# Optimization experiments

Hardware: AMD Instinct MI355X
Metric: run time of the kernel (lower is better)

Reference implementation:

```python
import jax, jax.numpy as jnp
import numpy as np

P = 8  # patch size
EPS = 1e-6

def ln2d(x, w, b):
    # LayerNorm over channel dim (dim=1), biased variance
    m = x.mean(1, keepdims=True)
    v = jnp.var(x, axis=1, keepdims=True)
    return (x - m) / jnp.sqrt(v + EPS) * w + b

def conv1x1(x, w, b=None):
    y = jnp.einsum('bchw,oc->bohw', x, w)
    if b is not None:
        y = y + b[None, :, None, None]
    return y

def dwconv3(x, w):
    # depthwise 3x3, padding=1; w: (C,1,3,3)
    return jax.lax.conv_general_dilated(
        x, w, window_strides=(1, 1), padding='SAME',
        feature_group_count=x.shape[1],
        dimension_numbers=('NCHW', 'OIHW', 'NCHW'))

def to_patches(x):
    B, C, H, W = x.shape
    x = x.reshape(B, C, H // P, P, W // P, P)
    return x.transpose(0, 1, 2, 4, 3, 5)  # b c h w p1 p2

def from_patches(x):
    B, C, h, w, p1, p2 = x.shape
    return x.transpose(0, 1, 2, 4, 3, 5).reshape(B, C, h * p1, w * p2)

def setup_inputs() -> dict:
    key = jax.random.key(0)
    ks = jax.random.split(key, 20)
    dim = 128
    dw = dim * 2          # 256
    ffn = dim * 2         # 256
    B, H, W = 2, 256, 256
    s = lambda k, shape, scale=0.05: jax.random.normal(k, shape, jnp.float32) * scale
    return {
        'x': jax.random.normal(ks[0], (B, dim, H, W), jnp.float32),
        'norm1_w': jnp.ones((1, dim, 1, 1), jnp.float32),
        'norm1_b': jnp.zeros((1, dim, 1, 1), jnp.float32),
        'w_h1': s(ks[1], (dw * 3, dim)),
        'w_dw1': s(ks[2], (dw * 3, 1, 3, 3)),
        'norm2_w': jnp.ones((1, dw, 1, 1), jnp.float32),
        'norm2_b': jnp.zeros((1, dw, 1, 1), jnp.float32),
        'w_p1': s(ks[3], (dim, dw)),
        'norm3_w': jnp.ones((1, dim, 1, 1), jnp.float32),
        'norm3_b': jnp.zeros((1, dim, 1, 1), jnp.float32),
        'w_h2': s(ks[4], (ffn, dim)),
        'b_h2': s(ks[5], (ffn,)),
        'w_dw2': s(ks[6], (ffn, 1, 3, 3)),
        'w_p2': s(ks[7], (dim, ffn // 2)),
        'scale1': s(ks[8], (1, dim, 1, 1), 0.01),
        'scale2': s(ks[9], (1, dim, 1, 1), 0.01),
    }

def reference(x, norm1_w, norm1_b, w_h1, w_dw1, norm2_w, norm2_b, w_p1,
              norm3_w, norm3_b, w_h2, b_h2, w_dw2, w_p2, scale1, scale2):
    identity = x
    h = ln2d(x, norm1_w, norm1_b)
    hidden = conv1x1(h, w_h1)
    qkv = dwconv3(hidden, w_dw1)
    q, k, v = jnp.split(qkv, 3, axis=1)
    # patch-wise FFT attention
    q_fft = jnp.fft.rfft2(to_patches(q).astype(jnp.float32), axes=(-2, -1))
    k_fft = jnp.fft.rfft2(to_patches(k).astype(jnp.float32), axes=(-2, -1))
    attn = jnp.fft.irfft2(q_fft * k_fft, s=(P, P), axes=(-2, -1))
    attn = from_patches(attn)
    attn = ln2d(attn, norm2_w, norm2_b)
    out = conv1x1(v * attn, w_p1)
    x = identity + out * scale1
    # FFN branch
    identity = x
    h = ln2d(x, norm3_w, norm3_b)
    h = conv1x1(h, w_h2, b_h2)
    h = dwconv3(h, w_dw2)
    h1, h2 = jnp.split(h, 2, axis=1)
    h = conv1x1(h1 * h2, w_p2)
    return identity + h * scale2
```

## Files before the change

kernel.cpp:

```cpp
#include <hip/hip_runtime.h>

typedef unsigned short u16;
typedef unsigned int u32;
typedef __attribute__((ext_vector_type(8))) short bf16x8;
typedef __attribute__((ext_vector_type(4))) float f32x4;

#define HW 65536

__device__ __forceinline__ float bf2f(u32 v) { return __uint_as_float(v << 16); }
__device__ __forceinline__ u16 f2bf(float f) {
  u32 u = __float_as_uint(f);
  u += 0x7fffu + ((u >> 16) & 1u);
  return (u16)(u >> 16);
}

__device__ __forceinline__ float dot2bf(u32 a, u32 b, float d) {
  asm("v_dot2_f32_bf16 %0, %1, %2, %0" : "+v"(d) : "v"(a), "v"(b));
  return d;
}

__device__ __forceinline__ void unpack8(uint4 u, float r[8]) {
  r[0] = bf2f(u.x & 0xffffu); r[1] = bf2f(u.x >> 16);
  r[2] = bf2f(u.y & 0xffffu); r[3] = bf2f(u.y >> 16);
  r[4] = bf2f(u.z & 0xffffu); r[5] = bf2f(u.z >> 16);
  r[6] = bf2f(u.w & 0xffffu); r[7] = bf2f(u.w >> 16);
}

__global__ __launch_bounds__(256)
void wprep_k(const float* __restrict__ wh1, const float* __restrict__ wp1,
             const float* __restrict__ wh2, u16* __restrict__ S)
{
  int i = blockIdx.x * 256 + threadIdx.x;
  if (i < 98304) {
    int j = i & 7, row = (i >> 3) & 127, kc = (i >> 10) & 15, mt = i >> 14;
    S[i] = f2bf(wh1[(mt * 128 + row) * 128 + kc * 8 + j]);
  } else if (i < 131072) {
    int k = i - 98304;
    int j = k & 7, row = (k >> 3) & 127, chl = (k >> 10) & 3, c0c = k >> 12;
    S[i] = f2bf(wp1[row * 256 + c0c * 32 + chl * 8 + j]);
  } else if (i < 163840) {
    int k = i - 131072;
    int j = k & 7, row = (k >> 3) & 127, kc = (k >> 10) & 15, mt = k >> 14;
    S[i] = f2bf(wh2[(mt * 128 + row) * 128 + kc * 8 + j]);
  }
}

__global__ __launch_bounds__(256, 2)
void ln1_k(const float* __restrict__ x, const float* __restrict__ gw,
           const float* __restrict__ gb, u16* __restrict__ y)
{
  __shared__ float xt[128][128];
  __shared__ float stm[128], str[128];
  int n0g = blockIdx.x << 7;
  int b = n0g >> 16;
  int p0 = n0g & (HW - 1);
  const float* xb = x + (size_t)b * 128 * HW + p0;
  u16* yb = y + (size_t)b * 128 * HW + p0;
  int t = threadIdx.x;
#pragma unroll
  for (int it = 0; it < 16; ++it) {
    int idx = t + it * 256;
    int ch = idx >> 5;
    int p4 = (idx & 31) << 2;
    *(float4*)&xt[ch][p4] = *(const float4*)(xb + (size_t)ch * HW + p4);
  }
  __syncthreads();
  if (t < 128) {
    float s = 0.f, q = 0.f;
    for (int c = 0; c < 128; ++c) {
      float a = xt[c][t];
      s += a; q += a * a;
    }
    const float inv = 1.0f / 128.0f;
    float m = s * inv;
    stm[t] = m;
    str[t] = rsqrtf(fmaxf(q * inv - m * m, 0.f) + 1e-6f);
  }
  __syncthreads();
  int p2 = (t & 63) << 1;
  int c0 = t >> 6;
  float m0 = stm[p2], r0 = str[p2], m1 = stm[p2 + 1], r1 = str[p2 + 1];
#pragma unroll
  for (int k = 0; k < 32; ++k) {
    int c = c0 + k * 4;
    float w = gw[c], bb = gb[c];
    float a = (xt[c][p2] - m0) * r0 * w + bb;
    float d = (xt[c][p2 + 1] - m1) * r1 * w + bb;
    *(u32*)(yb + (size_t)c * HW + p2) = (u32)f2bf(a) | ((u32)f2bf(d) << 16);
  }
}

__device__ __forceinline__ void gatherB(const u16* __restrict__ src,
                                        uint4& e, uint4& o)
{
  u32 w0 = *(const u32*)(src);
  u32 w1 = *(const u32*)(src + HW);
  u32 w2 = *(const u32*)(src + 2 * HW);
  u32 w3 = *(const u32*)(src + 3 * HW);
  u32 w4 = *(const u32*)(src + 4 * HW);
  u32 w5 = *(const u32*)(src + 5 * HW);
  u32 w6 = *(const u32*)(src + 6 * HW);
  u32 w7 = *(const u32*)(src + 7 * HW);
  e.x = (w0 & 0xffffu) | (w1 << 16);
  e.y = (w2 & 0xffffu) | (w3 << 16);
  e.z = (w4 & 0xffffu) | (w5 << 16);
  e.w = (w6 & 0xffffu) | (w7 << 16);
  o.x = (w0 >> 16) | (w1 & 0xffff0000u);
  o.y = (w2 >> 16) | (w3 & 0xffff0000u);
  o.z = (w4 >> 16) | (w5 & 0xffff0000u);
  o.w = (w6 >> 16) | (w7 & 0xffff0000u);
}

template <int AUXF32, int OUTF32>
__global__ __launch_bounds__(256, 2)
void gemm_k(const float* __restrict__ Wt, const u16* __restrict__ X,
            void* __restrict__ Yv, const void* __restrict__ aux,
            const float* __restrict__ scale, int M, int K, int xbatch)
{
  __shared__ __align__(16) u16 As[4][128][8];
  __shared__ __align__(16) u16 Bs[4][128][8];
  int mtiles = M >> 7;
  int mt = blockIdx.x % mtiles;
  int ntile = blockIdx.x / mtiles;
  int n0g = ntile << 7;
  int b = n0g >> 16;
  int p0 = n0g & (HW - 1);
  int o0 = mt << 7;
  const u16* Xb = X + (size_t)b * xbatch * HW;
  int t = threadIdx.x;
  int lane = t & 63, wv = t >> 6;
  int rb = (wv & 1) << 6, cb = (wv >> 1) << 6;
  int qd = lane >> 4, ln = lane & 15;
  f32x4 acc[4][4] = {};
  for (int c0 = 0; c0 < K; c0 += 32) {
#pragma unroll
    for (int it = 0; it < 2; ++it) {
      int tt = t + it * 256;
      int row = tt >> 2, ch = tt & 3;
      const float* wsrc = Wt + (size_t)(o0 + row) * K + c0 + ch * 8;
      uint4 pk;
      pk.x = (u32)f2bf(wsrc[0]) | ((u32)f2bf(wsrc[1]) << 16);
      pk.y = (u32)f2bf(wsrc[2]) | ((u32)f2bf(wsrc[3]) << 16);
      pk.z = (u32)f2bf(wsrc[4]) | ((u32)f2bf(wsrc[5]) << 16);
      pk.w = (u32)f2bf(wsrc[6]) | ((u32)f2bf(wsrc[7]) << 16);
      *(uint4*)&As[ch][row][0] = pk;
    }
    {
      int pp = (t & 63) << 1;
      int kc = t >> 6;
      const u16* src = Xb + (size_t)(c0 + kc * 8) * HW + p0 + pp;
      uint4 e, o;
      gatherB(src, e, o);
      *(uint4*)&Bs[kc][pp][0] = e;
      *(uint4*)&Bs[kc][pp + 1][0] = o;
    }
    __syncthreads();
    bf16x8 af[4], bfv[4];
#pragma unroll
    for (int i = 0; i < 4; ++i) {
      af[i] = *(const bf16x8*)&As[qd][rb + i * 16 + ln][0];
      bfv[i] = *(const bf16x8*)&Bs[qd][cb + i * 16 + ln][0];
    }
#pragma unroll
    for (int i = 0; i < 4; ++i)
#pragma unroll
      for (int j = 0; j < 4; ++j)
        acc[i][j] = __builtin_amdgcn_mfma_f32_16x16x32_bf16(af[i], bfv[j],
                                                            acc[i][j], 0, 0, 0);
    __syncthreads();
  }
  size_t ybase = (size_t)b * M * HW;
#pragma unroll
  for (int i = 0; i < 4; ++i) {
    int obase = o0 + rb + i * 16 + qd * 4;
#pragma unroll
    for (int j = 0; j < 4; ++j) {
      int p = p0 + cb + j * 16 + ln;
#pragma unroll
      for (int rr = 0; rr < 4; ++rr) {
        int o = obase + rr;
        size_t idx = ybase + (size_t)o * HW + p;
        float v = acc[i][j][rr];
        float r = AUXF32 ? ((const float*)aux)[idx]
                         : bf2f((u32)((const u16*)aux)[idx]);
        v = r + v * scale[o];
        if (OUTF32) ((float*)Yv)[idx] = v;
        else        ((u16*)Yv)[idx] = f2bf(v);
      }
    }
  }
}

__global__ __launch_bounds__(256, 2)
void lngemm_k(const u16* __restrict__ Wbf, const u16* __restrict__ X,
              u16* __restrict__ Y, const float* __restrict__ aux,
              const float* __restrict__ scale, const float* __restrict__ gw,
              const float* __restrict__ gb)
{
  __shared__ __align__(16) u16 At[32][128][8];
  __shared__ __align__(16) u16 As[4][128][8];
  __shared__ float stm[128], str[128];
  int n0g = blockIdx.x << 7;
  int b = n0g >> 16;
  int p0 = n0g & (HW - 1);
  const u16* Xb = X + (size_t)b * 768 * HW;
  int t = threadIdx.x;
  int lane = t & 63, wv = t >> 6;
  int rb = (wv & 1) << 6, cb = (wv >> 1) << 6;
  int qd = lane >> 4, ln = lane & 15;
#pragma unroll
  for (int it = 0; it < 8; ++it) {
    int kc = (t >> 6) + it * 4;
    int pp = (t & 63) << 1;
    const u16* src = Xb + (size_t)(kc * 8) * HW + p0 + pp;
    uint4 e, o;
    gatherB(src, e, o);
    *(uint4*)&At[kc][pp][0] = e;
    *(uint4*)&At[kc][pp + 1][0] = o;
  }
  __syncthreads();
  if (t < 128) {
    float s0 = 0.f, q0 = 0.f;
    for (int cg = 0; cg < 128; ++cg) {
      u32 u = *(const u32*)&At[cg >> 2][t][(cg & 3) << 1];
      float a = bf2f(u & 0xffffu);
      s0 += a; q0 += a * a;
      float d = bf2f(u >> 16);
      s0 += d; q0 += d * d;
    }
    const float inv = 1.0f / 256.0f;
    float m0 = s0 * inv;
    stm[t] = m0;
    str[t] = rsqrtf(fmaxf(q0 * inv - m0 * m0, 0.f) + 1e-6f);
  }
  __syncthreads();
  f32x4 acc[4][4] = {};
  for (int c0 = 0; c0 < 256; c0 += 32) {
    {
      const uint4* wsrc = (const uint4*)(Wbf + (size_t)(c0 >> 5) * 4096);
      ((uint4*)As)[t] = wsrc[t];
      ((uint4*)As)[t + 256] = wsrc[t + 256];
    }
    {
      int kcg = (c0 >> 3) + (t >> 6);
      int pp = (t & 63) << 1;
      const u16* vsrc = Xb + (size_t)(512 + kcg * 8) * HW + p0 + pp;
      uint4 ve, vo;
      gatherB(vsrc, ve, vo);
      float w8[8], b8[8];
#pragma unroll
      for (int j = 0; j < 8; ++j) {
        w8[j] = gw[kcg * 8 + j];
        b8[j] = gb[kcg * 8 + j];
      }
      float m0 = stm[pp], r0 = str[pp];
      float m1 = stm[pp + 1], r1 = str[pp + 1];
      uint4 e = *(const uint4*)&At[kcg][pp][0];
      uint4 o = *(const uint4*)&At[kcg][pp + 1][0];
      const u32* ew = (const u32*)&e;
      const u32* ow = (const u32*)&o;
      const u32* vew = (const u32*)&ve;
      const u32* vow = (const u32*)&vo;
      u32 re[4], ro[4];
#pragma unroll
      for (int j = 0; j < 4; ++j) {
        float a0 = ((bf2f(ew[j] & 0xffffu) - m0) * r0 * w8[2 * j] + b8[2 * j]) *
                   bf2f(vew[j] & 0xffffu);
        float a1 = ((bf2f(ew[j] >> 16) - m0) * r0 * w8[2 * j + 1] + b8[2 * j + 1]) *
                   bf2f(vew[j] >> 16);
        re[j] = (u32)f2bf(a0) | ((u32)f2bf(a1) << 16);
        float d0 = ((bf2f(ow[j] & 0xffffu) - m1) * r1 * w8[2 * j] + b8[2 * j]) *
                   bf2f(vow[j] & 0xffffu);
        float d1 = ((bf2f(ow[j] >> 16) - m1) * r1 * w8[2 * j + 1] + b8[2 * j + 1]) *
                   bf2f(vow[j] >> 16);
        ro[j] = (u32)f2bf(d0) | ((u32)f2bf(d1) << 16);
      }
      *(uint4*)&At[kcg][pp][0] = *(const uint4*)re;
      *(uint4*)&At[kcg][pp + 1][0] = *(const uint4*)ro;
    }
    __syncthreads();
    bf16x8 af[4], bfv[4];
    int kb = c0 >> 3;
#pragma unroll
    for (int i = 0; i < 4; ++i) {
      af[i] = *(const bf16x8*)&As[qd][rb + i * 16 + ln][0];
      bfv[i] = *(const bf16x8*)&At[kb + qd][cb + i * 16 + ln][0];
    }
#pragma unroll
    for (int i = 0; i < 4; ++i)
#pragma unroll
      for (int j = 0; j < 4; ++j)
        acc[i][j] = __builtin_amdgcn_mfma_f32_16x16x32_bf16(af[i], bfv[j],
                                                            acc[i][j], 0, 0, 0);
    __syncthreads();
  }
  size_t ybase = (size_t)b * 128 * HW;
#pragma unroll
  for (int i = 0; i < 4; ++i) {
    int obase = rb + i * 16 + qd * 4;
#pragma unroll
    for (int j = 0; j < 4; ++j) {
      int p = p0 + cb + j * 16 + ln;
#pragma unroll
      for (int rr = 0; rr < 4; ++rr) {
        int o = obase + rr;
        size_t idx = ybase + (size_t)o * HW + p;
        float v = acc[i][j][rr];
        float r = aux[idx];
        Y[idx] = f2bf(r + v * scale[o]);
      }
    }
  }
}

template <int EPI>
__global__ __launch_bounds__(256, 2)
void gemmf_k(const u16* __restrict__ Wbf, const u16* __restrict__ X,
             u16* __restrict__ Y, const float* __restrict__ bias,
             int MT, int xbatch)
{
  __shared__ __align__(16) u16 Bs[16][128][8];
  __shared__ __align__(16) u16 As[16][128][8];
  int n0g = blockIdx.x << 7;
  int b = n0g >> 16;
  int p0 = n0g & (HW - 1);
  const u16* Xb = X + (size_t)b * xbatch * HW;
  int t = threadIdx.x;
  int lane = t & 63, wv = t >> 6;
  int rb = (wv & 1) << 6, cb = (wv >> 1) << 6;
  int qd = lane >> 4, ln = lane & 15;
#pragma unroll
  for (int it = 0; it < 4; ++it) {
    int tt = t + it * 256;
    int pp = (tt & 63) << 1;
    int kc = tt >> 6;
    const u16* src = Xb + (size_t)(kc * 8) * HW + p0 + pp;
    uint4 e, o;
    gatherB(src, e, o);
    *(uint4*)&Bs[kc][pp][0] = e;
    *(uint4*)&Bs[kc][pp + 1][0] = o;
  }
  int M = MT << 7;
  size_t ybase = (size_t)b * M * HW;
  for (int mt = 0; mt < MT; ++mt) {
    __syncthreads();
    {
      const uint4* wsrc = (const uint4*)(Wbf + (size_t)mt * 16384);
#pragma unroll
      for (int it = 0; it < 8; ++it)
        ((uint4*)As)[t + it * 256] = wsrc[t + it * 256];
    }
    __syncthreads();
    f32x4 acc[4][4] = {};
#pragma unroll
    for (int s = 0; s < 4; ++s) {
      bf16x8 af[4], bfv[4];
#pragma unroll
      for (int i = 0; i < 4; ++i) {
        af[i] = *(const bf16x8*)&As[s * 4 + qd][rb + i * 16 + ln][0];
        bfv[i] = *(const bf16x8*)&Bs[s * 4 + qd][cb + i * 16 + ln][0];
      }
#pragma unroll
      for (int i = 0; i < 4; ++i)
#pragma unroll
        for (int j = 0; j < 4; ++j)
          acc[i][j] = __builtin_amdgcn_mfma_f32_16x16x32_bf16(af[i], bfv[j],
                                                              acc[i][j], 0, 0, 0);
    }
    int o0 = mt << 7;
#pragma unroll
    for (int i = 0; i < 4; ++i) {
      int obase = o0 + rb + i * 16 + qd * 4;
#pragma unroll
      for (int j = 0; j < 4; ++j) {
        int p = p0 + cb + j * 16 + ln;
#pragma unroll
        for (int rr = 0; rr < 4; ++rr) {
          int o = obase + rr;
          float v = acc[i][j][rr];
          if (EPI == 1) v += bias[o];
          Y[ybase + (size_t)o * HW + p] = f2bf(v);
        }
      }
    }
  }
}

__global__ __launch_bounds__(256, 2)
void lngemmf_k(const u16* __restrict__ Wbf, const u16* __restrict__ X,
               u16* __restrict__ Y, const float* __restrict__ bias,
               const float* __restrict__ gw, const float* __restrict__ gb,
               int MT, int xbatch)
{
  __shared__ __align__(16) u16 Bs[16][128][8];
  __shared__ __align__(16) u16 As[16][128][8];
  __shared__ float stm[128], str[128];
  int n0g = blockIdx.x << 7;
  int b = n0g >> 16;
  int p0 = n0g & (HW - 1);
  const u16* Xb = X + (size_t)b * xbatch * HW;
  int t = threadIdx.x;
  int lane = t & 63, wv = t >> 6;
  int rb = (wv & 1) << 6, cb = (wv >> 1) << 6;
  int qd = lane >> 4, ln = lane & 15;
#pragma unroll
  for (int it = 0; it < 4; ++it) {
    int tt = t + it * 256;
    int pp = (tt & 63) << 1;
    int kc = tt >> 6;
    const u16* src = Xb + (size_t)(kc * 8) * HW + p0 + pp;
    uint4 e, o;
    gatherB(src, e, o);
    *(uint4*)&Bs[kc][pp][0] = e;
    *(uint4*)&Bs[kc][pp + 1][0] = o;
  }
  __syncthreads();
  if (t < 128) {
    float s = 0.f, q = 0.f;
    for (int kc = 0; kc < 16; ++kc) {
      float r8[8];
      unpack8(*(const uint4*)&Bs[kc][t][0], r8);
#pragma unroll
      for (int j = 0; j < 8; ++j) {
        float a = r8[j];
        s += a; q += a * a;
      }
    }
    const float inv = 1.0f / 128.0f;
    float m = s * inv;
    stm[t] = m;
    str[t] = rsqrtf(fmaxf(q * inv - m * m, 0.f) + 1e-6f);
  }
  __syncthreads();
  {
    int pp = (t & 63) << 1;
    float m0 = stm[pp], r0 = str[pp];
    float m1 = stm[pp + 1], r1 = str[pp + 1];
#pragma unroll
    for (int mth = 0; mth < 4; ++mth) {
      int kc = (t >> 6) + mth * 4;
      float w8[8], b8[8];
#pragma unroll
      for (int j = 0; j < 8; ++j) {
        w8[j] = gw[kc * 8 + j];
        b8[j] = gb[kc * 8 + j];
      }
      float e8[8], o8[8];
      unpack8(*(const uint4*)&Bs[kc][pp][0], e8);
      unpack8(*(const uint4*)&Bs[kc][pp + 1][0], o8);
      uint4 pe, po;
      u32* pew = (u32*)&pe;
      u32* pow = (u32*)&po;
#pragma unroll
      for (int j = 0; j < 4; ++j) {
        float a0 = (e8[2 * j] - m0) * r0 * w8[2 * j] + b8[2 * j];
        float a1 = (e8[2 * j + 1] - m0) * r0 * w8[2 * j + 1] + b8[2 * j + 1];
        pew[j] = (u32)f2bf(a0) | ((u32)f2bf(a1) << 16);
        float d0 = (o8[2 * j] - m1) * r1 * w8[2 * j] + b8[2 * j];
        float d1 = (o8[2 * j + 1] - m1) * r1 * w8[2 * j + 1] + b8[2 * j + 1];
        pow[j] = (u32)f2bf(d0) | ((u32)f2bf(d1) << 16);
      }
      *(uint4*)&Bs[kc][pp][0] = pe;
      *(uint4*)&Bs[kc][pp + 1][0] = po;
    }
  }
  int M = MT << 7;
  size_t ybase = (size_t)b * M * HW;
  for (int mt = 0; mt < MT; ++mt) {
    __syncthreads();
    {
      const uint4* wsrc = (const uint4*)(Wbf + (size_t)mt * 16384);
#pragma unroll
      for (int it = 0; it < 8; ++it)
        ((uint4*)As)[t + it * 256] = wsrc[t + it * 256];
    }
    __syncthreads();
    f32x4 acc[4][4] = {};
#pragma unroll
    for (int s = 0; s < 4; ++s) {
      bf16x8 af[4], bfv[4];
#pragma unroll
      for (int i = 0; i < 4; ++i) {
        af[i] = *(const bf16x8*)&As[s * 4 + qd][rb + i * 16 + ln][0];
        bfv[i] = *(const bf16x8*)&Bs[s * 4 + qd][cb + i * 16 + ln][0];
      }
#pragma unroll
      for (int i = 0; i < 4; ++i)
#pragma unroll
        for (int j = 0; j < 4; ++j)
          acc[i][j] = __builtin_amdgcn_mfma_f32_16x16x32_bf16(af[i], bfv[j],
                                                              acc[i][j], 0, 0, 0);
    }
    int o0 = mt << 7;
#pragma unroll
    for (int i = 0; i < 4; ++i) {
      int obase = o0 + rb + i * 16 + qd * 4;
#pragma unroll
      for (int j = 0; j < 4; ++j) {
        int p = p0 + cb + j * 16 + ln;
#pragma unroll
        for (int rr = 0; rr < 4; ++rr) {
          int o = obase + rr;
          Y[ybase + (size_t)o * HW + p] = f2bf(acc[i][j][rr] + bias[o]);
        }
      }
    }
  }
}

__device__ __forceinline__ void ldsrow(const u16* __restrict__ img, int h,
                                       int w0, float* r) {
  if ((unsigned)h > 255u) {
#pragma unroll
    for (int i = 0; i < 10; ++i) r[i] = 0.f;
    return;
  }
  const u16* rp = img + (h << 8) + w0;
  float c[8];
  unpack8(*(const uint4*)rp, c);
#pragma unroll
  for (int i = 0; i < 8; ++i) r[i + 1] = c[i];
  r[0] = (w0 > 0) ? bf2f((u32)rp[-1]) : 0.f;
  r[9] = (w0 < 248) ? bf2f((u32)rp[8]) : 0.f;
}

__global__ __launch_bounds__(1024)
void dwip_k(u16* __restrict__ buf, const float* __restrict__ wt, int C)
{
  __shared__ __align__(16) u16 img[65536];
  int bc = blockIdx.x;
  int c = bc % C;
  size_t base = (size_t)bc << 16;
  int t = threadIdx.x;
  uint4* simg = (uint4*)img;
  const uint4* gsrc = (const uint4*)(buf + base);
#pragma unroll
  for (int it = 0; it < 8; ++it)
    simg[it * 1024 + t] = gsrc[it * 1024 + t];
  float wg[9];
#pragma unroll
  for (int i = 0; i < 9; ++i) wg[i] = wt[c * 9 + i];
  __syncthreads();
  uint4* gdst = (uint4*)(buf + base);
  int col = t & 31;
  int w0 = col << 3;
  int h0 = (t >> 5) << 3;
  float r0[10], r1[10], r2[10];
  ldsrow(img, h0 - 1, w0, r0);
  ldsrow(img, h0,     w0, r1);
#pragma unroll
  for (int k = 0; k < 8; ++k) {
    int h = h0 + k;
    ldsrow(img, h + 1, w0, r2);
    float o[8];
#pragma unroll
    for (int j = 0; j < 8; ++j) {
      float s = 0.f;
#pragma unroll
      for (int dx = 0; dx < 3; ++dx)
        s += r0[j + dx] * wg[dx] + r1[j + dx] * wg[3 + dx] +
             r2[j + dx] * wg[6 + dx];
      o[j] = s;
    }
    uint4 pk;
    pk.x = (u32)f2bf(o[0]) | ((u32)f2bf(o[1]) << 16);
    pk.y = (u32)f2bf(o[2]) | ((u32)f2bf(o[3]) << 16);
    pk.z = (u32)f2bf(o[4]) | ((u32)f2bf(o[5]) << 16);
    pk.w = (u32)f2bf(o[6]) | ((u32)f2bf(o[7]) << 16);
    gdst[(h << 5) + col] = pk;
#pragma unroll
    for (int i = 0; i < 10; ++i) { r0[i] = r1[i]; r1[i] = r2[i]; }
  }
}

__device__ __forceinline__ void ldsrow2(const u16* __restrict__ img, int lr,
                                        int w0, float* r) {
  const u16* rp = img + (lr << 8) + w0;
  float c[8];
  unpack8(*(const uint4*)rp, c);
#pragma unroll
  for (int i = 0; i < 8; ++i) r[i + 1] = c[i];
  r[0] = (w0 > 0) ? bf2f((u32)rp[-1]) : 0.f;
  r[9] = (w0 < 248) ? bf2f((u32)rp[8]) : 0.f;
}

__global__ __launch_bounds__(1024)
void dwfuse_k(const u16* __restrict__ h4, const float* __restrict__ wt,
              u16* __restrict__ pr)
{
  __shared__ __align__(16) u16 img[33280];
  int bx = blockIdx.x;
  int b = bx >> 8;
  int c = (bx >> 1) & 127;
  int half = bx & 1;
  int h0 = half << 7;
  int t = threadIdx.x;
  float o1[32];
  size_t obase = ((size_t)((b << 7) + c) << 16);
  int col = t & 31;
  int w0 = col << 3;
  int l0 = (t >> 5) << 2;
#pragma unroll
  for (int pass = 0; pass < 2; ++pass) {
    int ch = c + pass * 128;
    size_t gbase = (size_t)((b << 8) + ch) << 16;
    __syncthreads();
    for (int idx = t; idx < 4160; idx += 1024) {
      int lr = idx >> 5, cl = idx & 31;
      int gh = h0 - 1 + lr;
      uint4 v = {0, 0, 0, 0};
      if ((unsigned)gh < 256u)
        v = *(const uint4*)(h4 + gbase + ((size_t)gh << 8) + cl * 8);
      *(uint4*)&img[(lr << 8) + cl * 8] = v;
    }
    float wg[9];
#pragma unroll
    for (int i = 0; i < 9; ++i) wg[i] = wt[ch * 9 + i];
    __syncthreads();
    float r0[10], r1[10], r2[10];
    ldsrow2(img, l0,     w0, r0);
    ldsrow2(img, l0 + 1, w0, r1);
#pragma unroll
    for (int k = 0; k < 4; ++k) {
      int lrr = l0 + k;
      ldsrow2(img, lrr + 2, w0, r2);
      float o[8];
#pragma unroll
      for (int j = 0; j < 8; ++j) {
        float s = 0.f;
#pragma unroll
        for (int dx = 0; dx < 3; ++dx)
          s += r0[j + dx] * wg[dx] + r1[j + dx] * wg[3 + dx] +
               r2[j + dx] * wg[6 + dx];
        o[j] = s;
      }
      if (pass == 0) {
#pragma unroll
        for (int j = 0; j < 8; ++j) o1[k * 8 + j] = o[j];
      } else {
        uint4 pk;
        pk.x = (u32)f2bf(o1[k*8+0] * o[0]) | ((u32)f2bf(o1[k*8+1] * o[1]) << 16);
        pk.y = (u32)f2bf(o1[k*8+2] * o[2]) | ((u32)f2bf(o1[k*8+3] * o[3]) << 16);
        pk.z = (u32)f2bf(o1[k*8+4] * o[4]) | ((u32)f2bf(o1[k*8+5] * o[5]) << 16);
        pk.w = (u32)f2bf(o1[k*8+6] * o[6]) | ((u32)f2bf(o1[k*8+7] * o[7]) << 16);
        *(uint4*)(pr + obase + ((size_t)(h0 + lrr) << 8) + w0) = pk;
      }
#pragma unroll
      for (int i = 0; i < 10; ++i) { r0[i] = r1[i]; r1[i] = r2[i]; }
    }
  }
}

__global__ __launch_bounds__(256)
void attn_k(u16* __restrict__ qkv)
{
  int wv = threadIdx.x >> 6, lane = threadIdx.x & 63;
  int task = blockIdx.x * 4 + wv;
  int b = task >> 12;
  int c = (task >> 4) & 255;
  int strip = task & 15;
  int pr = lane >> 5, pw = lane & 31;
  int row = (strip << 4) + (pr << 3);
  size_t qbase = ((size_t)(b * 768 + c) << 16) + ((size_t)row << 8) + pw * 8;
  size_t kbase = qbase + ((size_t)256 << 16);
  u32 qp[8][4];
  u32 ku[8][4];
#pragma unroll
  for (int i = 0; i < 8; ++i) {
    uint4 qv = *(const uint4*)(qkv + qbase + (i << 8));
    uint4 kv = *(const uint4*)(qkv + kbase + (i << 8));
    qp[i][0] = qv.x; qp[i][1] = qv.y; qp[i][2] = qv.z; qp[i][3] = qv.w;
    ku[i][0] = kv.x; ku[i][1] = kv.y; ku[i][2] = kv.z; ku[i][3] = kv.w;
  }
  u32 pk[8][8];
#pragma unroll
  for (int r = 0; r < 8; ++r)
#pragma unroll
    for (int n = 0; n < 8; ++n) {
      if (n & 1) {
        u32 x = ku[r][n >> 1];
        pk[r][n] = (x >> 16) | (x << 16);
      } else {
        pk[r][n] = (ku[r][n >> 1] & 0xffffu) |
                   (ku[r][((n + 7) & 7) >> 1] & 0xffff0000u);
      }
    }
#pragma unroll
  for (int m = 0; m < 8; ++m) {
    float a[8] = {};
#pragma unroll
    for (int i = 0; i < 8; ++i) {
      const int r = (m - i) & 7;
#pragma unroll
      for (int t = 0; t < 4; ++t) {
        const u32 q = qp[i][t];
#pragma unroll
        for (int n = 0; n < 8; ++n)
          a[n] = dot2bf(q, pk[r][(n - 2 * t) & 7], a[n]);
      }
    }
    uint4 pko;
    pko.x = (u32)f2bf(a[0]) | ((u32)f2bf(a[1]) << 16);
    pko.y = (u32)f2bf(a[2]) | ((u32)f2bf(a[3]) << 16);
    pko.z = (u32)f2bf(a[4]) | ((u32)f2bf(a[5]) << 16);
    pko.w = (u32)f2bf(a[6]) | ((u32)f2bf(a[7]) << 16);
    *(uint4*)(qkv + qbase + (m << 8)) = pko;
  }
}

extern "C" void kernel_launch(void* const* d_in, const int* in_sizes, int n_in,
                              void* d_out, int out_size, void* d_ws, size_t ws_size,
                              hipStream_t stream)
{
  (void)in_sizes; (void)n_in; (void)out_size; (void)ws_size;
  const float* x    = (const float*)d_in[0];
  const float* n1w  = (const float*)d_in[1];
  const float* n1b  = (const float*)d_in[2];
  const float* wh1  = (const float*)d_in[3];
  const float* wdw1 = (const float*)d_in[4];
  const float* n2w  = (const float*)d_in[5];
  const float* n2b  = (const float*)d_in[6];
  const float* wp1  = (const float*)d_in[7];
  const float* n3w  = (const float*)d_in[8];
  const float* n3b  = (const float*)d_in[9];
  const float* wh2  = (const float*)d_in[10];
  const float* bh2  = (const float*)d_in[11];
  const float* wdw2 = (const float*)d_in[12];
  const float* wp2  = (const float*)d_in[13];
  const float* sc1  = (const float*)d_in[14];
  const float* sc2  = (const float*)d_in[15];
  float* out = (float*)d_out;
  u16* ws = (u16*)d_ws;

  u16* A = ws;
  u16* B = ws + 100663296;
  u16* h4 = A + 16777216;
  u16* pr = A;
  u16* S = (u16*)d_out;

  wprep_k<<<640, 256, 0, stream>>>(wh1, wp1, wh2, S);
  ln1_k<<<1024, 256, 0, stream>>>(x, n1w, n1b, B);
  gemmf_k<0><<<1024, 256, 0, stream>>>(S, B, A, nullptr, 6, 128);
  dwip_k<<<1536, 1024, 0, stream>>>(A, wdw1, 768);
  attn_k<<<2048, 256, 0, stream>>>(A);
  lngemm_k<<<1024, 256, 0, stream>>>(S + 98304, A, B, x, sc1, n2w, n2b);
  lngemmf_k<<<1024, 256, 0, stream>>>(S + 131072, B, h4, bh2, n3w, n3b, 2, 128);
  dwfuse_k<<<512, 1024, 0, stream>>>(h4, wdw2, pr);
  gemm_k<0,1><<<1024, 256, 0, stream>>>(wp2, pr, out, B, sc2, 128, 128, 128);
}
```

Baseline: 454.2 us.

## Halve dwconv LDS footprint and pre-convert final GEMM weights to bf16

```diff
diff --git a/kernel.cpp b/kernel.cpp
--- a/kernel.cpp
+++ b/kernel.cpp
@@ -43,6 +43,14 @@
     int j = k & 7, row = (k >> 3) & 127, kc = (k >> 10) & 15, mt = k >> 14;
     S[i] = f2bf(wh2[(mt * 128 + row) * 128 + kc * 8 + j]);
   }
+}
+
+__global__ __launch_bounds__(256)
+void wprep2_k(const float* __restrict__ wp2, u16* __restrict__ S3)
+{
+  int i = blockIdx.x * 256 + threadIdx.x;
+  int j = i & 7, row = (i >> 3) & 127, chl = (i >> 10) & 3, c0c = i >> 12;
+  S3[i] = f2bf(wp2[row * 128 + c0c * 32 + chl * 8 + j]);
 }
 
 __global__ __launch_bounds__(256, 2)
@@ -111,39 +119,27 @@
   o.w = (w6 >> 16) | (w7 & 0xffff0000u);
 }
 
-template <int AUXF32, int OUTF32>
 __global__ __launch_bounds__(256, 2)
-void gemm_k(const float* __restrict__ Wt, const u16* __restrict__ X,
-            void* __restrict__ Yv, const void* __restrict__ aux,
-            const float* __restrict__ scale, int M, int K, int xbatch)
+void gemmw_k(const u16* __restrict__ Wbf, const u16* __restrict__ X,
+             float* __restrict__ Y, const u16* __restrict__ aux,
+             const float* __restrict__ scale)
 {
   __shared__ __align__(16) u16 As[4][128][8];
   __shared__ __align__(16) u16 Bs[4][128][8];
-  int mtiles = M >> 7;
-  int mt = blockIdx.x % mtiles;
-  int ntile = blockIdx.x / mtiles;
-  int n0g = ntile << 7;
+  int n0g = blockIdx.x << 7;
   int b = n0g >> 16;
   int p0 = n0g & (HW - 1);
-  int o0 = mt << 7;
-  const u16* Xb = X + (size_t)b * xbatch * HW;
+  const u16* Xb = X + (size_t)b * 128 * HW;
   int t = threadIdx.x;
   int lane = t & 63, wv = t >> 6;
   int rb = (wv & 1) << 6, cb = (wv >> 1) << 6;
   int qd = lane >> 4, ln = lane & 15;
   f32x4 acc[4][4] = {};
-  for (int c0 = 0; c0 < K; c0 += 32) {
-#pragma unroll
-    for (int it = 0; it < 2; ++it) {
-      int tt = t + it * 256;
-      int row = tt >> 2, ch = tt & 3;
-      const float* wsrc = Wt + (size_t)(o0 + row) * K + c0 + ch * 8;
-      uint4 pk;
-      pk.x = (u32)f2bf(wsrc[0]) | ((u32)f2bf(wsrc[1]) << 16);
-      pk.y = (u32)f2bf(wsrc[2]) | ((u32)f2bf(wsrc[3]) << 16);
-      pk.z = (u32)f2bf(wsrc[4]) | ((u32)f2bf(wsrc[5]) << 16);
-      pk.w = (u32)f2bf(wsrc[6]) | ((u32)f2bf(wsrc[7]) << 16);
-      *(uint4*)&As[ch][row][0] = pk;
+  for (int c0 = 0; c0 < 128; c0 += 32) {
+    {
+      const uint4* wsrc = (const uint4*)(Wbf + (size_t)(c0 >> 5) * 4096);
+      ((uint4*)As)[t] = wsrc[t];
+      ((uint4*)As)[t + 256] = wsrc[t + 256];
     }
     {
       int pp = (t & 63) << 1;
@@ -169,10 +165,10 @@
                                                             acc[i][j], 0, 0, 0);
     __syncthreads();
   }
-  size_t ybase = (size_t)b * M * HW;
+  size_t ybase = (size_t)b * 128 * HW;
 #pragma unroll
   for (int i = 0; i < 4; ++i) {
-    int obase = o0 + rb + i * 16 + qd * 4;
+    int obase = rb + i * 16 + qd * 4;
 #pragma unroll
     for (int j = 0; j < 4; ++j) {
       int p = p0 + cb + j * 16 + ln;
@@ -180,12 +176,8 @@
       for (int rr = 0; rr < 4; ++rr) {
         int o = obase + rr;
         size_t idx = ybase + (size_t)o * HW + p;
-        float v = acc[i][j][rr];
-        float r = AUXF32 ? ((const float*)aux)[idx]
-                         : bf2f((u32)((const u16*)aux)[idx]);
-        v = r + v * scale[o];
-        if (OUTF32) ((float*)Yv)[idx] = v;
-        else        ((u16*)Yv)[idx] = f2bf(v);
+        float r = bf2f((u32)aux[idx]);
+        Y[idx] = r + acc[i][j][rr] * scale[o];
       }
     }
   }
@@ -508,14 +500,14 @@
   }
 }
 
-__device__ __forceinline__ void ldsrow(const u16* __restrict__ img, int h,
-                                       int w0, float* r) {
-  if ((unsigned)h > 255u) {
+__device__ __forceinline__ void ldsrowS(const u16* __restrict__ img, int slot,
+                                        int w0, float* r) {
+  if (slot < 0) {
 #pragma unroll
     for (int i = 0; i < 10; ++i) r[i] = 0.f;
     return;
   }
-  const u16* rp = img + (h << 8) + w0;
+  const u16* rp = img + (slot << 8) + w0;
   float c[8];
   unpack8(*(const uint4*)rp, c);
 #pragma unroll
@@ -524,52 +516,97 @@
   r[9] = (w0 < 248) ? bf2f((u32)rp[8]) : 0.f;
 }
 
+__device__ __forceinline__ int smap(int g) {
+  return (g == 127) ? 127 : (g == 128) ? 128 : g - 129;
+}
+
 __global__ __launch_bounds__(1024)
 void dwip_k(u16* __restrict__ buf, const float* __restrict__ wt, int C)
 {
-  __shared__ __align__(16) u16 img[65536];
+  __shared__ __align__(16) uint4 sl[4128];
+  const u16* L = (const u16*)sl;
   int bc = blockIdx.x;
   int c = bc % C;
-  size_t base = (size_t)bc << 16;
   int t = threadIdx.x;
-  uint4* simg = (uint4*)img;
-  const uint4* gsrc = (const uint4*)(buf + base);
-#pragma unroll
-  for (int it = 0; it < 8; ++it)
-    simg[it * 1024 + t] = gsrc[it * 1024 + t];
   float wg[9];
 #pragma unroll
   for (int i = 0; i < 9; ++i) wg[i] = wt[c * 9 + i];
-  __syncthreads();
-  uint4* gdst = (uint4*)(buf + base);
+  uint4* Gch = (uint4*)(buf + ((size_t)bc << 16));
+  for (int idx = t; idx < 4128; idx += 1024)
+    sl[idx] = Gch[idx];
+  __syncthreads();
+  uint4 st[4];
+#pragma unroll
+  for (int r = 0; r < 4; ++r) {
+    int idx = t + r * 1024;
+    if (idx < 4064) st[r] = Gch[4128 + idx];
+  }
   int col = t & 31;
   int w0 = col << 3;
-  int h0 = (t >> 5) << 3;
-  float r0[10], r1[10], r2[10];
-  ldsrow(img, h0 - 1, w0, r0);
-  ldsrow(img, h0,     w0, r1);
-#pragma unroll
-  for (int k = 0; k < 8; ++k) {
-    int h = h0 + k;
-    ldsrow(img, h + 1, w0, r2);
-    float o[8];
-#pragma unroll
-    for (int j = 0; j < 8; ++j) {
-      float s = 0.f;
-#pragma unroll
-      for (int dx = 0; dx < 3; ++dx)
-        s += r0[j + dx] * wg[dx] + r1[j + dx] * wg[3 + dx] +
-             r2[j + dx] * wg[6 + dx];
-      o[j] = s;
-    }
-    uint4 pk;
-    pk.x = (u32)f2bf(o[0]) | ((u32)f2bf(o[1]) << 16);
-    pk.y = (u32)f2bf(o[2]) | ((u32)f2bf(o[3]) << 16);
-    pk.z = (u32)f2bf(o[4]) | ((u32)f2bf(o[5]) << 16);
-    pk.w = (u32)f2bf(o[6]) | ((u32)f2bf(o[7]) << 16);
-    gdst[(h << 5) + col] = pk;
-#pragma unroll
-    for (int i = 0; i < 10; ++i) { r0[i] = r1[i]; r1[i] = r2[i]; }
+  int h0 = (t >> 5) << 2;
+  {
+    float r0[10], r1[10], r2[10];
+    ldsrowS(L, h0 - 1, w0, r0);
+    ldsrowS(L, h0, w0, r1);
+#pragma unroll
+    for (int k = 0; k < 4; ++k) {
+      int h = h0 + k;
+      ldsrowS(L, h + 1, w0, r2);
+      float o[8];
+#pragma unroll
+      for (int j = 0; j < 8; ++j) {
+        float s = 0.f;
+#pragma unroll
+        for (int dx = 0; dx < 3; ++dx)
+          s += r0[j + dx] * wg[dx] + r1[j + dx] * wg[3 + dx] +
+               r2[j + dx] * wg[6 + dx];
+        o[j] = s;
+      }
+      uint4 pk;
+      pk.x = (u32)f2bf(o[0]) | ((u32)f2bf(o[1]) << 16);
+      pk.y = (u32)f2bf(o[2]) | ((u32)f2bf(o[3]) << 16);
+      pk.z = (u32)f2bf(o[4]) | ((u32)f2bf(o[5]) << 16);
+      pk.w = (u32)f2bf(o[6]) | ((u32)f2bf(o[7]) << 16);
+      Gch[(h << 5) + col] = pk;
+#pragma unroll
+      for (int i = 0; i < 10; ++i) { r0[i] = r1[i]; r1[i] = r2[i]; }
+    }
+  }
+  __syncthreads();
+#pragma unroll
+  for (int r = 0; r < 4; ++r) {
+    int idx = t + r * 1024;
+    if (idx < 4064) sl[idx] = st[r];
+  }
+  __syncthreads();
+  {
+    int R0 = 128 + h0;
+    float r0[10], r1[10], r2[10];
+    ldsrowS(L, smap(R0 - 1), w0, r0);
+    ldsrowS(L, smap(R0), w0, r1);
+#pragma unroll
+    for (int k = 0; k < 4; ++k) {
+      int R = R0 + k;
+      ldsrowS(L, (R == 255) ? -1 : smap(R + 1), w0, r2);
+      float o[8];
+#pragma unroll
+      for (int j = 0; j < 8; ++j) {
+        float s = 0.f;
+#pragma unroll
+        for (int dx = 0; dx < 3; ++dx)
+          s += r0[j + dx] * wg[dx] + r1[j + dx] * wg[3 + dx] +
+               r2[j + dx] * wg[6 + dx];
+        o[j] = s;
+      }
+      uint4 pk;
+      pk.x = (u32)f2bf(o[0]) | ((u32)f2bf(o[1]) << 16);
+      pk.y = (u32)f2bf(o[2]) | ((u32)f2bf(o[3]) << 16);
+      pk.z = (u32)f2bf(o[4]) | ((u32)f2bf(o[5]) << 16);
+      pk.w = (u32)f2bf(o[6]) | ((u32)f2bf(o[7]) << 16);
+      Gch[(R << 5) + col] = pk;
+#pragma unroll
+      for (int i = 0; i < 10; ++i) { r0[i] = r1[i]; r1[i] = r2[i]; }
+    }
   }
 }
 
@@ -737,6 +774,7 @@
   u16* h4 = A + 16777216;
   u16* pr = A;
   u16* S = (u16*)d_out;
+  u16* S3 = A + 16777216;
 
   wprep_k<<<640, 256, 0, stream>>>(wh1, wp1, wh2, S);
   ln1_k<<<1024, 256, 0, stream>>>(x, n1w, n1b, B);
@@ -746,5 +784,6 @@
   lngemm_k<<<1024, 256, 0, stream>>>(S + 98304, A, B, x, sc1, n2w, n2b);
   lngemmf_k<<<1024, 256, 0, stream>>>(S + 131072, B, h4, bh2, n3w, n3b, 2, 128);
   dwfuse_k<<<512, 1024, 0, stream>>>(h4, wdw2, pr);
-  gemm_k<0,1><<<1024, 256, 0, stream>>>(wp2, pr, out, B, sc2, 128, 128, 128);
-}
+  wprep2_k<<<64, 256, 0, stream>>>(wp2, S3);
+  gemmw_k<<<1024, 256, 0, stream>>>(S3, pr, out, B, sc2);
+}
```

After: 498.8 us. 9.8% more time.

## Fuse q/k depthwise conv with patch FFT-attention in one kernel

Applied to the files above, without the earlier changes.

```diff
diff --git a/kernel.cpp b/kernel.cpp
--- a/kernel.cpp
+++ b/kernel.cpp
@@ -43,6 +43,18 @@
     int j = k & 7, row = (k >> 3) & 127, kc = (k >> 10) & 15, mt = k >> 14;
     S[i] = f2bf(wh2[(mt * 128 + row) * 128 + kc * 8 + j]);
   }
+}
+
+__global__ __launch_bounds__(256)
+void qhalo_k(const u16* __restrict__ A, u16* __restrict__ Hq)
+{
+  int i = blockIdx.x * 256 + threadIdx.x;
+  int ch = i >> 6;
+  int off = i & 63;
+  int b = ch >> 8, cq = ch & 255;
+  const uint4* src = (const uint4*)(A + ((size_t)(b * 768 + cq) << 16) +
+                                    (127 << 8));
+  ((uint4*)Hq)[i] = src[off];
 }
 
 __global__ __launch_bounds__(256, 2)
@@ -508,6 +520,17 @@
   }
 }
 
+__device__ __forceinline__ void ldsrow2(const u16* __restrict__ img, int lr,
+                                        int w0, float* r) {
+  const u16* rp = img + (lr << 8) + w0;
+  float c[8];
+  unpack8(*(const uint4*)rp, c);
+#pragma unroll
+  for (int i = 0; i < 8; ++i) r[i + 1] = c[i];
+  r[0] = (w0 > 0) ? bf2f((u32)rp[-1]) : 0.f;
+  r[9] = (w0 < 248) ? bf2f((u32)rp[8]) : 0.f;
+}
+
 __device__ __forceinline__ void ldsrow(const u16* __restrict__ img, int h,
                                        int w0, float* r) {
   if ((unsigned)h > 255u) {
@@ -525,12 +548,13 @@
 }
 
 __global__ __launch_bounds__(1024)
-void dwip_k(u16* __restrict__ buf, const float* __restrict__ wt, int C)
+void dwipv_k(u16* __restrict__ buf, const float* __restrict__ wt)
 {
   __shared__ __align__(16) u16 img[65536];
-  int bc = blockIdx.x;
-  int c = bc % C;
-  size_t base = (size_t)bc << 16;
+  int bx = blockIdx.x;
+  int b = bx >> 8;
+  int c = 512 + (bx & 255);
+  size_t base = (size_t)(b * 768 + c) << 16;
   int t = threadIdx.x;
   uint4* simg = (uint4*)img;
   const uint4* gsrc = (const uint4*)(buf + base);
@@ -573,15 +597,143 @@
   }
 }
 
-__device__ __forceinline__ void ldsrow2(const u16* __restrict__ img, int lr,
-                                        int w0, float* r) {
-  const u16* rp = img + (lr << 8) + w0;
-  float c[8];
-  unpack8(*(const uint4*)rp, c);
-#pragma unroll
-  for (int i = 0; i < 8; ++i) r[i + 1] = c[i];
-  r[0] = (w0 > 0) ? bf2f((u32)rp[-1]) : 0.f;
-  r[9] = (w0 < 248) ? bf2f((u32)rp[8]) : 0.f;
+__global__ __launch_bounds__(1024)
+void qkattn_k(u16* __restrict__ A, const float* __restrict__ wt,
+              const u16* __restrict__ Hq)
+{
+  __shared__ __align__(16) u16 qin[33280];
+  __shared__ __align__(16) u16 kin[33280];
+  int bx = blockIdx.x;
+  int b = bx >> 9;
+  int c = (bx >> 1) & 255;
+  int half = bx & 1;
+  int h0 = half << 7;
+  int t = threadIdx.x;
+  u16* Gq = A + ((size_t)(b * 768 + c) << 16);
+  const u16* Gk = A + ((size_t)(b * 768 + 256 + c) << 16);
+  const u16* Hc = Hq + ((size_t)(b * 256 + c) << 9);
+  for (int idx = t; idx < 4160; idx += 1024) {
+    int lr = idx >> 5, cl = idx & 31;
+    int gh = h0 - 1 + lr;
+    uint4 qv = {0, 0, 0, 0}, kv = {0, 0, 0, 0};
+    if ((unsigned)gh < 256u) {
+      bool other = (half == 0) ? (gh == 128) : (gh == 127);
+      if (other) qv = *(const uint4*)(Hc + ((gh - 127) << 8) + cl * 8);
+      else       qv = *(const uint4*)(Gq + ((size_t)gh << 8) + cl * 8);
+      kv = *(const uint4*)(Gk + ((size_t)gh << 8) + cl * 8);
+    }
+    *(uint4*)&qin[(lr << 8) + cl * 8] = qv;
+    *(uint4*)&kin[(lr << 8) + cl * 8] = kv;
+  }
+  float wq[9], wk[9];
+#pragma unroll
+  for (int i = 0; i < 9; ++i) {
+    wq[i] = wt[c * 9 + i];
+    wk[i] = wt[(256 + c) * 9 + i];
+  }
+  __syncthreads();
+  int col = t & 31, w0 = col << 3, l0 = (t >> 5) << 2;
+  uint4 qres[4], kres[4];
+  {
+    float r0[10], r1[10], r2[10];
+    ldsrow2(qin, l0,     w0, r0);
+    ldsrow2(qin, l0 + 1, w0, r1);
+#pragma unroll
+    for (int kk = 0; kk < 4; ++kk) {
+      ldsrow2(qin, l0 + 2 + kk, w0, r2);
+      float o[8];
+#pragma unroll
+      for (int j = 0; j < 8; ++j) {
+        float s = 0.f;
+#pragma unroll
+        for (int dx = 0; dx < 3; ++dx)
+          s += r0[j + dx] * wq[dx] + r1[j + dx] * wq[3 + dx] +
+               r2[j + dx] * wq[6 + dx];
+        o[j] = s;
+      }
+      qres[kk].x = (u32)f2bf(o[0]) | ((u32)f2bf(o[1]) << 16);
+      qres[kk].y = (u32)f2bf(o[2]) | ((u32)f2bf(o[3]) << 16);
+      qres[kk].z = (u32)f2bf(o[4]) | ((u32)f2bf(o[5]) << 16);
+      qres[kk].w = (u32)f2bf(o[6]) | ((u32)f2bf(o[7]) << 16);
+#pragma unroll
+      for (int i = 0; i < 10; ++i) { r0[i] = r1[i]; r1[i] = r2[i]; }
+    }
+  }
+  {
+    float r0[10], r1[10], r2[10];
+    ldsrow2(kin, l0,     w0, r0);
+    ldsrow2(kin, l0 + 1, w0, r1);
+#pragma unroll
+    for (int kk = 0; kk < 4; ++kk) {
+      ldsrow2(kin, l0 + 2 + kk, w0, r2);
+      float o[8];
+#pragma unroll
+      for (int j = 0; j < 8; ++j) {
+        float s = 0.f;
+#pragma unroll
+        for (int dx = 0; dx < 3; ++dx)
+          s += r0[j + dx] * wk[dx] + r1[j + dx] * wk[3 + dx] +
+               r2[j + dx] * wk[6 + dx];
+        o[j] = s;
+      }
+      kres[kk].x = (u32)f2bf(o[0]) | ((u32)f2bf(o[1]) << 16);
+      kres[kk].y = (u32)f2bf(o[2]) | ((u32)f2bf(o[3]) << 16);
+      kres[kk].z = (u32)f2bf(o[4]) | ((u32)f2bf(o[5]) << 16);
+      kres[kk].w = (u32)f2bf(o[6]) | ((u32)f2bf(o[7]) << 16);
+#pragma unroll
+      for (int i = 0; i < 10; ++i) { r0[i] = r1[i]; r1[i] = r2[i]; }
+    }
+  }
+  __syncthreads();
+  uint4* qc = (uint4*)qin;
+  uint4* kc = (uint4*)kin;
+#pragma unroll
+  for (int kk = 0; kk < 4; ++kk) {
+    qc[((l0 + kk) << 5) + col] = qres[kk];
+    kc[((l0 + kk) << 5) + col] = kres[kk];
+  }
+  __syncthreads();
+  int patch = t >> 1, mh = t & 1;
+  int pr = patch >> 5, pc = patch & 31;
+  u32 qp[8][4];
+  u32 pk[8][8];
+#pragma unroll
+  for (int i = 0; i < 8; ++i) {
+    uint4 qv = qc[((pr * 8 + i) << 5) + pc];
+    qp[i][0] = qv.x; qp[i][1] = qv.y; qp[i][2] = qv.z; qp[i][3] = qv.w;
+    uint4 kv = kc[((pr * 8 + i) << 5) + pc];
+    u32 k0 = kv.x, k1 = kv.y, k2 = kv.z, k3 = kv.w;
+    pk[i][0] = (k0 & 0xffffu) | (k3 & 0xffff0000u);
+    pk[i][1] = (k0 >> 16) | (k0 << 16);
+    pk[i][2] = (k1 & 0xffffu) | (k0 & 0xffff0000u);
+    pk[i][3] = (k1 >> 16) | (k1 << 16);
+    pk[i][4] = (k2 & 0xffffu) | (k1 & 0xffff0000u);
+    pk[i][5] = (k2 >> 16) | (k2 << 16);
+    pk[i][6] = (k3 & 0xffffu) | (k2 & 0xffff0000u);
+    pk[i][7] = (k3 >> 16) | (k3 << 16);
+  }
+#pragma unroll
+  for (int mi = 0; mi < 4; ++mi) {
+    int m = mh * 4 + mi;
+    float a[8] = {};
+#pragma unroll
+    for (int i = 0; i < 8; ++i) {
+      const int r = (m - i) & 7;
+#pragma unroll
+      for (int tt = 0; tt < 4; ++tt) {
+        const u32 q = qp[i][tt];
+#pragma unroll
+        for (int n = 0; n < 8; ++n)
+          a[n] = dot2bf(q, pk[r][(n - 2 * tt) & 7], a[n]);
+      }
+    }
+    uint4 pko;
+    pko.x = (u32)f2bf(a[0]) | ((u32)f2bf(a[1]) << 16);
+    pko.y = (u32)f2bf(a[2]) | ((u32)f2bf(a[3]) << 16);
+    pko.z = (u32)f2bf(a[4]) | ((u32)f2bf(a[5]) << 16);
+    pko.w = (u32)f2bf(a[6]) | ((u32)f2bf(a[7]) << 16);
+    *(uint4*)(Gq + ((size_t)(h0 + pr * 8 + m) << 8) + pc * 8) = pko;
+  }
 }
 
 __global__ __launch_bounds__(1024)
@@ -648,63 +800,6 @@
 #pragma unroll
       for (int i = 0; i < 10; ++i) { r0[i] = r1[i]; r1[i] = r2[i]; }
     }
-  }
-}
-
-__global__ __launch_bounds__(256)
-void attn_k(u16* __restrict__ qkv)
-{
-  int wv = threadIdx.x >> 6, lane = threadIdx.x & 63;
-  int task = blockIdx.x * 4 + wv;
-  int b = task >> 12;
-  int c = (task >> 4) & 255;
-  int strip = task & 15;
-  int pr = lane >> 5, pw = lane & 31;
-  int row = (strip << 4) + (pr << 3);
-  size_t qbase = ((size_t)(b * 768 + c) << 16) + ((size_t)row << 8) + pw * 8;
-  size_t kbase = qbase + ((size_t)256 << 16);
-  u32 qp[8][4];
-  u32 ku[8][4];
-#pragma unroll
-  for (int i = 0; i < 8; ++i) {
-    uint4 qv = *(const uint4*)(qkv + qbase + (i << 8));
-    uint4 kv = *(const uint4*)(qkv + kbase + (i << 8));
-    qp[i][0] = qv.x; qp[i][1] = qv.y; qp[i][2] = qv.z; qp[i][3] = qv.w;
-    ku[i][0] = kv.x; ku[i][1] = kv.y; ku[i][2] = kv.z; ku[i][3] = kv.w;
-  }
-  u32 pk[8][8];
-#pragma unroll
-  for (int r = 0; r < 8; ++r)
-#pragma unroll
-    for (int n = 0; n < 8; ++n) {
-      if (n & 1) {
-        u32 x = ku[r][n >> 1];
-        pk[r][n] = (x >> 16) | (x << 16);
-      } else {
-        pk[r][n] = (ku[r][n >> 1] & 0xffffu) |
-                   (ku[r][((n + 7) & 7) >> 1] & 0xffff0000u);
-      }
-    }
-#pragma unroll
-  for (int m = 0; m < 8; ++m) {
-    float a[8] = {};
-#pragma unroll
-    for (int i = 0; i < 8; ++i) {
-      const int r = (m - i) & 7;
-#pragma unroll
-      for (int t = 0; t < 4; ++t) {
-        const u32 q = qp[i][t];
-#pragma unroll
-        for (int n = 0; n < 8; ++n)
-          a[n] = dot2bf(q, pk[r][(n - 2 * t) & 7], a[n]);
-      }
-    }
-    uint4 pko;
-    pko.x = (u32)f2bf(a[0]) | ((u32)f2bf(a[1]) << 16);
-    pko.y = (u32)f2bf(a[2]) | ((u32)f2bf(a[3]) << 16);
-    pko.z = (u32)f2bf(a[4]) | ((u32)f2bf(a[5]) << 16);
-    pko.w = (u32)f2bf(a[6]) | ((u32)f2bf(a[7]) << 16);
-    *(uint4*)(qkv + qbase + (m << 8)) = pko;
   }
 }
 
@@ -737,12 +832,14 @@
   u16* h4 = A + 16777216;
   u16* pr = A;
   u16* S = (u16*)d_out;
+  u16* Hq = S + 163840;
 
   wprep_k<<<640, 256, 0, stream>>>(wh1, wp1, wh2, S);
   ln1_k<<<1024, 256, 0, stream>>>(x, n1w, n1b, B);
   gemmf_k<0><<<1024, 256, 0, stream>>>(S, B, A, nullptr, 6, 128);
-  dwip_k<<<1536, 1024, 0, stream>>>(A, wdw1, 768);
-  attn_k<<<2048, 256, 0, stream>>>(A);
+  qhalo_k<<<128, 256, 0, stream>>>(A, Hq);
+  dwipv_k<<<512, 1024, 0, stream>>>(A, wdw1);
+  qkattn_k<<<1024, 1024, 0, stream>>>(A, wdw1, Hq);
   lngemm_k<<<1024, 256, 0, stream>>>(S + 98304, A, B, x, sc1, n2w, n2b);
   lngemmf_k<<<1024, 256, 0, stream>>>(S + 131072, B, h4, bh2, n3w, n3b, 2, 128);
   dwfuse_k<<<512, 1024, 0, stream>>>(h4, wdw2, pr);
```

Result: slower. 637.8 us (+40.4%).
